# Kernel tuning notes

Measured on AMD Instinct MI355X. Metric: run time of the kernel, lower is better.

The kernel has to match this reference:

```python
import jax, jax.numpy as jnp
from jax import lax
import numpy as np

N = 32768
IN_PLANES = 64
OUT_PLANES = 128
STRIDE = 4
NSAMPLE = 16
EPS = 1e-5


def setup_inputs() -> dict:
    key = jax.random.key(0)
    kp, kx, kw = jax.random.split(key, 3)
    p = jax.random.normal(kp, (N, 3), dtype=jnp.float32)
    x = jax.random.normal(kx, (N, IN_PLANES), dtype=jnp.float32)
    o = jnp.array([N], dtype=jnp.int32)  # batch offsets, passed through unused
    W = jax.random.normal(kw, (3 + IN_PLANES, OUT_PLANES), dtype=jnp.float32) * 0.05
    gamma = jnp.ones((OUT_PLANES,), dtype=jnp.float32)
    beta = jnp.zeros((OUT_PLANES,), dtype=jnp.float32)
    return {"p": p, "x": x, "o": o, "W": W, "gamma": gamma, "beta": beta,
            "stride": STRIDE, "nsample": NSAMPLE}


def fps_indices(p, m):
    # Faithful to the source's furthest_point_sampling: each step picks the
    # argmax of squared distance to the LAST selected point (NOT min over all
    # selected points). Start index fixed to 0 for determinism (source uses a
    # random start).
    def step(last, _):
        d = jnp.sum((p - p[last]) ** 2, axis=1)
        nxt = jnp.argmax(d).astype(jnp.int32)
        return nxt, nxt
    _, rest = lax.scan(step, jnp.int32(0), None, length=m - 1)
    return jnp.concatenate([jnp.zeros((1,), jnp.int32), rest])


def reference(p, x, o, W, gamma, beta, stride, nsample):
    m = p.shape[0] // stride
    fps_idx = fps_indices(p, m)
    new_p = p[fps_idx]                                     # [M,3]

    # exact kNN (KDTree query equivalent): squared euclidean distances [M,N]
    d2 = (jnp.sum(new_p * new_p, axis=1, keepdims=True)
          - 2.0 * new_p @ p.T
          + jnp.sum(p * p, axis=1)[None, :])
    knn = lax.top_k(-lax.stop_gradient(d2), nsample)[1]    # [M,K] nearest indices

    # group: cat(absolute grouped xyz, grouped features) -> [M,K,3+C]
    g = jnp.concatenate([p[knn], x[knn]], axis=-1)
    h = jnp.einsum('mkc,cd->mkd', g, W)                    # linear, [M,K,OUT]

    # BatchNorm1d (training mode, batch statistics) over (M,K) per channel
    mean = jnp.mean(h, axis=(0, 1))
    var = jnp.var(h, axis=(0, 1))
    h = (h - mean) * lax.rsqrt(var + EPS) * gamma + beta
    h = jax.nn.relu(h)

    x_out = jnp.max(h, axis=1)                             # MaxPool1d over nsample
    return new_p, x_out
```

## Files before the change

### kernel.cpp

```cpp
#include <hip/hip_runtime.h>

#define N_PTS 32768
#define M_PTS 8192
#define C_IN  64
#define C_OUT 128
#define KNN   16
#define GDIM  67
#define BN_EPS 1e-5f
#define MAXC  64

#define OFF_FPS   0u
#define OFF_META  32768u
#define OFF_KNN   33024u
#define OFF_CAND  557312u
#define OFF_HBUF  1605888u
#define OFF_UROW  2129920u

typedef unsigned int uint32;
typedef unsigned long long uint64;

__device__ __forceinline__ int slot_count(int s, int nun, int cs, int cl, int M) {
    if (s < cs) return 1;
    const int E = M - nun;
    const int base = E / cl, rem = E % cl;
    const int start = (nun - cs) % cl;
    int off = (s - cs) - start; if (off < 0) off += cl;
    return 1 + base + (off < rem ? 1 : 0);
}

__device__ __forceinline__ uint32 dist_key(float d) {
    uint32 u = __float_as_uint(d);
    return (u & 0x80000000u) ? ~u : (u | 0x80000000u);
}

__global__ void __launch_bounds__(1024) fps_chain_kernel(const float* __restrict__ p,
                                                         int* __restrict__ fps,
                                                         int* __restrict__ meta) {
    __shared__ int   s_chain[M_PTS];
    __shared__ float wv_d[16];
    __shared__ int   wv_i[16];
    __shared__ int s_last, s_done, s_cs, s_win, s_found;
    const int tid  = threadIdx.x;
    const int lane = tid & 63;
    const int wid  = tid >> 6;

    if (tid == 0) { s_chain[0] = 0; s_last = 0; s_done = 0; s_cs = 0; }
    __syncthreads();

    int t = 1;
    while (t < M_PTS) {
        const int last = s_last;
        const float qx = p[3*last], qy = p[3*last+1], qz = p[3*last+2];
        float bd = -1.0f; int bi = 0;
#pragma unroll
        for (int j = 0; j < 32; ++j) {
            const int i = tid + (j << 10);
            float dx = __fsub_rn(p[3*i],   qx);
            float dy = __fsub_rn(p[3*i+1], qy);
            float dz = __fsub_rn(p[3*i+2], qz);
            float d  = __fadd_rn(__fadd_rn(__fmul_rn(dx,dx), __fmul_rn(dy,dy)),
                                 __fmul_rn(dz,dz));
            if (d > bd) { bd = d; bi = i; }
        }
#pragma unroll
        for (int off = 32; off > 0; off >>= 1) {
            float od = __shfl_xor(bd, off);
            int   oi = __shfl_xor(bi, off);
            if (od > bd || (od == bd && oi < bi)) { bd = od; bi = oi; }
        }
        if (lane == 0) { wv_d[wid] = bd; wv_i[wid] = bi; }
        __syncthreads();
        if (wid == 0) {
            float rd = (lane < 16) ? wv_d[lane] : -1.0f;
            int   ri = (lane < 16) ? wv_i[lane] : 0x7fffffff;
#pragma unroll
            for (int off = 8; off > 0; off >>= 1) {
                float od = __shfl_xor(rd, off);
                int   oi = __shfl_xor(ri, off);
                if (od > rd || (od == rd && oi < ri)) { rd = od; ri = oi; }
            }
            if (lane == 0) { s_win = ri; s_found = -1; }
        }
        __syncthreads();
        const int nxt = s_win;
        for (int i = tid; i < t; i += 1024)
            if (s_chain[i] == nxt) s_found = i;
        __syncthreads();
        if (tid == 0) {
            if (s_found >= 0) { s_cs = s_found; s_done = 1; }
            else { s_chain[t] = nxt; s_last = nxt; }
        }
        __syncthreads();
        if (s_done) break;
        ++t;
    }

    if (tid == 0) {
        if (s_done) { meta[0] = t; meta[1] = s_cs; meta[2] = t - s_cs; }
        else        { meta[0] = M_PTS; meta[1] = 0; meta[2] = 1; }
    }
    const int nun = s_done ? t : M_PTS;
    for (int i = tid; i < nun; i += 1024) fps[i] = s_chain[i];
}

__global__ void __launch_bounds__(1024) knn_part_kernel(const float* __restrict__ p,
                                                        const int* __restrict__ fps,
                                                        const int* __restrict__ meta,
                                                        uint64* __restrict__ cand,
                                                        float* __restrict__ newp) {
    const int tid   = threadIdx.x;
    const int lane  = tid & 63;
    const int wid   = tid >> 6;
    const int slice = blockIdx.x & 7;
    const int c0    = blockIdx.x >> 3;
    const int nun   = meta[0];
    const int cs    = meta[1], cl = meta[2];

    for (int e = blockIdx.x * 1024 + tid; e < M_PTS; e += gridDim.x * 1024) {
        const int sl = (e < nun) ? e : cs + (e - cs) % cl;
        const int id = fps[sl];
        newp[3*e]   = p[3*id];
        newp[3*e+1] = p[3*id+1];
        newp[3*e+2] = p[3*id+2];
    }

    for (int c = c0; c < nun && c < MAXC; c += 16) {
        const int cpt = fps[c];
        const float qx = p[3*cpt], qy = p[3*cpt+1], qz = p[3*cpt+2];
        const int base = slice << 12;

        uint64 pk4[4];
#pragma unroll
        for (int j = 0; j < 4; ++j) {
            const int i = base + tid + (j << 10);
            float dx = p[3*i]   - qx;
            float dy = p[3*i+1] - qy;
            float dz = p[3*i+2] - qz;
            float d  = fmaf(dx, dx, fmaf(dy, dy, dz*dz));
            pk4[j] = ((uint64)dist_key(d) << 32) | (uint32)i;
        }

        uint64 lastv = 0ull;
        uint64* out = cand + ((size_t)c << 11) + (slice << 8) + (wid << 4);
        for (int r = 0; r < KNN; ++r) {
            uint64 m = ~0ull;
#pragma unroll
            for (int j = 0; j < 4; ++j) {
                const uint64 v = pk4[j];
                if (v > lastv && v < m) m = v;
            }
#pragma unroll
            for (int off = 32; off > 0; off >>= 1) {
                uint64 o = __shfl_xor(m, off);
                if (o < m) m = o;
            }
            if (lane == 0) out[r] = m;
            lastv = m;
        }
    }
}

__global__ void __launch_bounds__(128) hstats_kernel(const float* __restrict__ p,
                                                     const float* __restrict__ x,
                                                     const float* __restrict__ W,
                                                     const int* __restrict__ meta,
                                                     const uint64* __restrict__ cand,
                                                     float* __restrict__ hbuf) {
    const int c = blockIdx.x >> 4;
    const int k = blockIdx.x & 15;
    const int nun = meta[0];
    if (c >= nun || c >= MAXC) return;
    const int tid  = threadIdx.x;
    const int lane = tid & 63;
    const int wv   = tid >> 6;

    __shared__ uint64 wmin[2];
    __shared__ uint64 s_win;
    __shared__ float  gbuf[GDIM + 1];

    uint64 kc[16];
    const uint64* src = cand + ((size_t)c << 11);
#pragma unroll
    for (int j = 0; j < 16; ++j) kc[j] = src[tid + (j << 7)];

    uint64 lastv = 0ull;
    for (int r = 0; r <= k; ++r) {
        uint64 m = ~0ull;
#pragma unroll
        for (int j = 0; j < 16; ++j) {
            const uint64 v = kc[j];
            if (v > lastv && v < m) m = v;
        }
#pragma unroll
        for (int off = 32; off > 0; off >>= 1) {
            uint64 o = __shfl_xor(m, off);
            if (o < m) m = o;
        }
        if (lane == 0) wmin[wv] = m;
        __syncthreads();
        if (tid == 0) s_win = wmin[0] < wmin[1] ? wmin[0] : wmin[1];
        __syncthreads();
        lastv = s_win;
    }
    const int pt = (int)(lastv & 0xFFFFFFFFull);

    if (tid < GDIM) gbuf[tid] = (tid < 3) ? p[3*pt + tid] : x[(pt << 6) + tid - 3];
    __syncthreads();
    float a = 0.f;
#pragma unroll
    for (int cc = 0; cc < GDIM; ++cc)
        a = fmaf(gbuf[cc], W[cc*C_OUT + tid], a);
    hbuf[(size_t)((c << 4) + k)*C_OUT + tid] = a;
}

__global__ void __launch_bounds__(128) finurow_kernel(const float* __restrict__ p,
                                                      const float* __restrict__ x,
                                                      const float* __restrict__ W,
                                                      const float* __restrict__ gamma,
                                                      const float* __restrict__ beta,
                                                      const int* __restrict__ fps,
                                                      const int* __restrict__ meta,
                                                      const float* __restrict__ hbuf,
                                                      int* __restrict__ knn,
                                                      float* __restrict__ urow) {
    const int tid  = threadIdx.x;
    const int lane = tid & 63;
    const int wv   = tid >> 6;
    const int nun  = meta[0], cs = meta[1], cl = meta[2];
    const int cmax = (nun < MAXC) ? nun : MAXC;

    __shared__ uint64 wmin[2];
    __shared__ uint64 s_win;
    __shared__ float  gbuf[GDIM + 1];

    float s_sum = 0.f, s_sq = 0.f;

    for (int c = 0; c < cmax; ++c) {
        float ls = 0.f, lq = 0.f;
        const float* hb = hbuf + ((size_t)c << 4)*C_OUT;
#pragma unroll
        for (int k = 0; k < KNN; ++k) {
            const float a = hb[k*C_OUT + tid];
            ls += a;
            lq = fmaf(a, a, lq);
        }
        const float cf = (float)slot_count(c, nun, cs, cl, M_PTS);
        s_sum = fmaf(cf, ls, s_sum);
        s_sq  = fmaf(cf, lq, s_sq);
    }
    for (int c = MAXC; c < nun; ++c) {
        const int cpt = fps[c];
        const float qx = p[3*cpt], qy = p[3*cpt+1], qz = p[3*cpt+2];
        uint64 lastv = 0ull;
        for (int r = 0; r < KNN; ++r) {
            uint64 m = ~0ull;
            for (int i = tid; i < N_PTS; i += 128) {
                float dx = p[3*i]   - qx;
                float dy = p[3*i+1] - qy;
                float dz = p[3*i+2] - qz;
                float d  = fmaf(dx, dx, fmaf(dy, dy, dz*dz));
                uint64 v = ((uint64)dist_key(d) << 32) | (uint32)i;
                if (v > lastv && v < m) m = v;
            }
#pragma unroll
            for (int off = 32; off > 0; off >>= 1) {
                uint64 o = __shfl_xor(m, off);
                if (o < m) m = o;
            }
            if (lane == 0) wmin[wv] = m;
            __syncthreads();
            if (tid == 0) {
                uint64 w = wmin[0] < wmin[1] ? wmin[0] : wmin[1];
                s_win = w;
                knn[c*KNN + r] = (int)(w & 0xFFFFFFFFull);
            }
            __syncthreads();
            lastv = s_win;
        }
        float ls = 0.f, lq = 0.f;
#pragma unroll
        for (int k = 0; k < KNN; ++k) {
            const int pt = knn[c*KNN + k];
            if (tid < GDIM) gbuf[tid] = (tid < 3) ? p[3*pt + tid]
                                                  : x[(pt << 6) + tid - 3];
            __syncthreads();
            float a = 0.f;
#pragma unroll
            for (int cc = 0; cc < GDIM; ++cc)
                a = fmaf(gbuf[cc], W[cc*C_OUT + tid], a);
            ls += a;
            lq = fmaf(a, a, lq);
            __syncthreads();
        }
        const float cf = (float)slot_count(c, nun, cs, cl, M_PTS);
        s_sum = fmaf(cf, ls, s_sum);
        s_sq  = fmaf(cf, lq, s_sq);
    }

    const float inv  = 1.0f / (float)(M_PTS * KNN);
    const float mean = s_sum * inv;
    const float var  = s_sq * inv - mean*mean;
    const float sc   = gamma[tid] * rsqrtf(var + BN_EPS);
    const float sh   = fmaf(-mean, sc, beta[tid]);

    for (int c = 0; c < cmax; ++c) {
        const float* hb = hbuf + ((size_t)c << 4)*C_OUT;
        float mx = 0.f;
#pragma unroll
        for (int k = 0; k < KNN; ++k)
            mx = fmaxf(mx, fmaf(hb[k*C_OUT + tid], sc, sh));
        urow[(size_t)c*C_OUT + tid] = mx;
    }
    for (int c = MAXC; c < nun; ++c) {
        float mx = 0.f;
#pragma unroll
        for (int k = 0; k < KNN; ++k) {
            const int pt = knn[c*KNN + k];
            if (tid < GDIM) gbuf[tid] = (tid < 3) ? p[3*pt + tid]
                                                  : x[(pt << 6) + tid - 3];
            __syncthreads();
            float a = 0.f;
#pragma unroll
            for (int cc = 0; cc < GDIM; ++cc)
                a = fmaf(gbuf[cc], W[cc*C_OUT + tid], a);
            mx = fmaxf(mx, fmaf(a, sc, sh));
            __syncthreads();
        }
        urow[(size_t)c*C_OUT + tid] = mx;
    }
}

__global__ void __launch_bounds__(256) bcast_kernel(const int* __restrict__ meta,
                                                    const float* __restrict__ urow,
                                                    float* __restrict__ xout) {
    const int nun = meta[0], cs = meta[1], cl = meta[2];
    const int idx = blockIdx.x * 256 + threadIdx.x;
    const int m = idx >> 5;
    if (m >= M_PTS) return;
    const int c4 = idx & 31;
    const int sl = (m < nun) ? m : cs + (m - cs) % cl;
    float4 v = ((const float4*)urow)[(size_t)sl*32 + c4];
    ((float4*)xout)[(size_t)m*32 + c4] = v;
}

extern "C" void kernel_launch(void* const* d_in, const int* in_sizes, int n_in,
                              void* d_out, int out_size, void* d_ws, size_t ws_size,
                              hipStream_t stream) {
    (void)in_sizes; (void)n_in; (void)out_size; (void)ws_size;
    const float* p     = (const float*)d_in[0];
    const float* x     = (const float*)d_in[1];
    const float* W     = (const float*)d_in[3];
    const float* gamma = (const float*)d_in[4];
    const float* beta  = (const float*)d_in[5];

    float* out  = (float*)d_out;
    float* newp = out;
    float* xout = out + M_PTS * 3;

    char* ws = (char*)d_ws;
    int*    fps   = (int*)   (ws + OFF_FPS);
    int*    meta  = (int*)   (ws + OFF_META);
    int*    knn   = (int*)   (ws + OFF_KNN);
    uint64* cand  = (uint64*)(ws + OFF_CAND);
    float*  hbuf  = (float*) (ws + OFF_HBUF);
    float*  urow  = (float*) (ws + OFF_UROW);

    fps_chain_kernel<<<1, 1024, 0, stream>>>(p, fps, meta);
    knn_part_kernel <<<128, 1024, 0, stream>>>(p, fps, meta, cand, newp);
    hstats_kernel   <<<MAXC*KNN, 128, 0, stream>>>(p, x, W, meta, cand, hbuf);
    finurow_kernel  <<<1, 128, 0, stream>>>(p, x, W, gamma, beta, fps, meta,
                                            hbuf, knn, urow);
    bcast_kernel    <<<M_PTS*32/256, 256, 0, stream>>>(meta, urow, xout);
}
```

Baseline: 58.04 us.

## Vectorize point loads and fuse BN-finalize with broadcast into one grid kernel

Measured after the change: 51.87 us. -10.6%, faster.

```diff
diff --git a/kernel.cpp b/kernel.cpp
--- a/kernel.cpp
+++ b/kernel.cpp
@@ -14,7 +14,6 @@
 #define OFF_KNN   33024u
 #define OFF_CAND  557312u
 #define OFF_HBUF  1605888u
-#define OFF_UROW  2129920u
 
 typedef unsigned int uint32;
 typedef unsigned long long uint64;
@@ -43,6 +42,7 @@
     const int tid  = threadIdx.x;
     const int lane = tid & 63;
     const int wid  = tid >> 6;
+    const float4* p4 = (const float4*)p;
 
     if (tid == 0) { s_chain[0] = 0; s_last = 0; s_done = 0; s_cs = 0; }
     __syncthreads();
@@ -53,14 +53,24 @@
         const float qx = p[3*last], qy = p[3*last+1], qz = p[3*last+2];
         float bd = -1.0f; int bi = 0;
 #pragma unroll
-        for (int j = 0; j < 32; ++j) {
-            const int i = tid + (j << 10);
-            float dx = __fsub_rn(p[3*i],   qx);
-            float dy = __fsub_rn(p[3*i+1], qy);
-            float dz = __fsub_rn(p[3*i+2], qz);
-            float d  = __fadd_rn(__fadd_rn(__fmul_rn(dx,dx), __fmul_rn(dy,dy)),
-                                 __fmul_rn(dz,dz));
-            if (d > bd) { bd = d; bi = i; }
+        for (int j = 0; j < 8; ++j) {
+            const int u = (j << 10) + tid;
+            const int b = u << 2;
+            const float4 f0 = p4[3*u];
+            const float4 f1 = p4[3*u + 1];
+            const float4 f2 = p4[3*u + 2];
+            const float xs[4] = {f0.x, f0.w, f1.z, f2.y};
+            const float ys[4] = {f0.y, f1.x, f1.w, f2.z};
+            const float zs[4] = {f0.z, f1.y, f2.x, f2.w};
+#pragma unroll
+            for (int q = 0; q < 4; ++q) {
+                float dx = __fsub_rn(xs[q], qx);
+                float dy = __fsub_rn(ys[q], qy);
+                float dz = __fsub_rn(zs[q], qz);
+                float d  = __fadd_rn(__fadd_rn(__fmul_rn(dx,dx), __fmul_rn(dy,dy)),
+                                     __fmul_rn(dz,dz));
+                if (d > bd) { bd = d; bi = b + q; }
+            }
         }
 #pragma unroll
         for (int off = 32; off > 0; off >>= 1) {
@@ -115,6 +125,7 @@
     const int c0    = blockIdx.x >> 3;
     const int nun   = meta[0];
     const int cs    = meta[1], cl = meta[2];
+    const float4* p4 = (const float4*)p;
 
     for (int e = blockIdx.x * 1024 + tid; e < M_PTS; e += gridDim.x * 1024) {
         const int sl = (e < nun) ? e : cs + (e - cs) % cl;
@@ -127,17 +138,21 @@
     for (int c = c0; c < nun && c < MAXC; c += 16) {
         const int cpt = fps[c];
         const float qx = p[3*cpt], qy = p[3*cpt+1], qz = p[3*cpt+2];
-        const int base = slice << 12;
+        const int bp = (slice << 12) + (tid << 2);
+        const int u0 = (slice * 3072) + 3*tid;
+        const float4 f0 = p4[u0], f1 = p4[u0+1], f2 = p4[u0+2];
+        const float xs[4] = {f0.x, f0.w, f1.z, f2.y};
+        const float ys[4] = {f0.y, f1.x, f1.w, f2.z};
+        const float zs[4] = {f0.z, f1.y, f2.x, f2.w};
 
         uint64 pk4[4];
 #pragma unroll
-        for (int j = 0; j < 4; ++j) {
-            const int i = base + tid + (j << 10);
-            float dx = p[3*i]   - qx;
-            float dy = p[3*i+1] - qy;
-            float dz = p[3*i+2] - qz;
+        for (int q = 0; q < 4; ++q) {
+            float dx = xs[q] - qx;
+            float dy = ys[q] - qy;
+            float dz = zs[q] - qz;
             float d  = fmaf(dx, dx, fmaf(dy, dy, dz*dz));
-            pk4[j] = ((uint64)dist_key(d) << 32) | (uint32)i;
+            pk4[q] = ((uint64)dist_key(d) << 32) | (uint32)(bp + q);
         }
 
         uint64 lastv = 0ull;
@@ -145,8 +160,8 @@
         for (int r = 0; r < KNN; ++r) {
             uint64 m = ~0ull;
 #pragma unroll
-            for (int j = 0; j < 4; ++j) {
-                const uint64 v = pk4[j];
+            for (int q = 0; q < 4; ++q) {
+                const uint64 v = pk4[q];
                 if (v > lastv && v < m) m = v;
             }
 #pragma unroll
@@ -213,40 +228,41 @@
     hbuf[(size_t)((c << 4) + k)*C_OUT + tid] = a;
 }
 
-__global__ void __launch_bounds__(128) finurow_kernel(const float* __restrict__ p,
-                                                      const float* __restrict__ x,
-                                                      const float* __restrict__ W,
-                                                      const float* __restrict__ gamma,
-                                                      const float* __restrict__ beta,
-                                                      const int* __restrict__ fps,
-                                                      const int* __restrict__ meta,
-                                                      const float* __restrict__ hbuf,
-                                                      int* __restrict__ knn,
-                                                      float* __restrict__ urow) {
-    const int tid  = threadIdx.x;
-    const int lane = tid & 63;
-    const int wv   = tid >> 6;
-    const int nun  = meta[0], cs = meta[1], cl = meta[2];
+__global__ void __launch_bounds__(256) outall_kernel(const float* __restrict__ p,
+                                                     const float* __restrict__ x,
+                                                     const float* __restrict__ W,
+                                                     const float* __restrict__ gamma,
+                                                     const float* __restrict__ beta,
+                                                     const int* __restrict__ fps,
+                                                     const int* __restrict__ meta,
+                                                     const float* __restrict__ hbuf,
+                                                     int* __restrict__ knn,
+                                                     float* __restrict__ xout) {
+    const int tid = threadIdx.x;
+    const int blk = blockIdx.x;
+    const int nun = meta[0], cs = meta[1], cl = meta[2];
     const int cmax = (nun < MAXC) ? nun : MAXC;
 
-    __shared__ uint64 wmin[2];
+    __shared__ float  ssc[128], ssh[128];
+    __shared__ float  gbuf[GDIM + 1];
+    __shared__ uint64 wred[4];
     __shared__ uint64 s_win;
-    __shared__ float  gbuf[GDIM + 1];
 
     float s_sum = 0.f, s_sq = 0.f;
-
-    for (int c = 0; c < cmax; ++c) {
-        float ls = 0.f, lq = 0.f;
-        const float* hb = hbuf + ((size_t)c << 4)*C_OUT;
-#pragma unroll
-        for (int k = 0; k < KNN; ++k) {
-            const float a = hb[k*C_OUT + tid];
-            ls += a;
-            lq = fmaf(a, a, lq);
-        }
-        const float cf = (float)slot_count(c, nun, cs, cl, M_PTS);
-        s_sum = fmaf(cf, ls, s_sum);
-        s_sq  = fmaf(cf, lq, s_sq);
+    if (tid < 128) {
+        for (int c = 0; c < cmax; ++c) {
+            const float* hb = hbuf + ((size_t)c << 4)*C_OUT;
+            float ls = 0.f, lq = 0.f;
+#pragma unroll
+            for (int k = 0; k < KNN; ++k) {
+                const float a = hb[k*C_OUT + tid];
+                ls += a;
+                lq = fmaf(a, a, lq);
+            }
+            const float cf = (float)slot_count(c, nun, cs, cl, M_PTS);
+            s_sum = fmaf(cf, ls, s_sum);
+            s_sq  = fmaf(cf, lq, s_sq);
+        }
     }
     for (int c = MAXC; c < nun; ++c) {
         const int cpt = fps[c];
@@ -254,7 +270,7 @@
         uint64 lastv = 0ull;
         for (int r = 0; r < KNN; ++r) {
             uint64 m = ~0ull;
-            for (int i = tid; i < N_PTS; i += 128) {
+            for (int i = tid; i < N_PTS; i += 256) {
                 float dx = p[3*i]   - qx;
                 float dy = p[3*i+1] - qy;
                 float dz = p[3*i+2] - qz;
@@ -267,12 +283,15 @@
                 uint64 o = __shfl_xor(m, off);
                 if (o < m) m = o;
             }
-            if (lane == 0) wmin[wv] = m;
+            if ((tid & 63) == 0) wred[tid >> 6] = m;
             __syncthreads();
             if (tid == 0) {
-                uint64 w = wmin[0] < wmin[1] ? wmin[0] : wmin[1];
+                uint64 w = wred[0];
+                if (wred[1] < w) w = wred[1];
+                if (wred[2] < w) w = wred[2];
+                if (wred[3] < w) w = wred[3];
                 s_win = w;
-                knn[c*KNN + r] = (int)(w & 0xFFFFFFFFull);
+                knn[(size_t)c*KNN + r] = (int)(w & 0xFFFFFFFFull);
             }
             __syncthreads();
             lastv = s_win;
@@ -280,67 +299,77 @@
         float ls = 0.f, lq = 0.f;
 #pragma unroll
         for (int k = 0; k < KNN; ++k) {
-            const int pt = knn[c*KNN + k];
+            const int pt = knn[(size_t)c*KNN + k];
             if (tid < GDIM) gbuf[tid] = (tid < 3) ? p[3*pt + tid]
                                                   : x[(pt << 6) + tid - 3];
             __syncthreads();
-            float a = 0.f;
-#pragma unroll
-            for (int cc = 0; cc < GDIM; ++cc)
-                a = fmaf(gbuf[cc], W[cc*C_OUT + tid], a);
-            ls += a;
-            lq = fmaf(a, a, lq);
+            if (tid < 128) {
+                float a = 0.f;
+#pragma unroll
+                for (int cc = 0; cc < GDIM; ++cc)
+                    a = fmaf(gbuf[cc], W[cc*C_OUT + tid], a);
+                ls += a;
+                lq = fmaf(a, a, lq);
+            }
             __syncthreads();
         }
-        const float cf = (float)slot_count(c, nun, cs, cl, M_PTS);
-        s_sum = fmaf(cf, ls, s_sum);
-        s_sq  = fmaf(cf, lq, s_sq);
-    }
-
-    const float inv  = 1.0f / (float)(M_PTS * KNN);
-    const float mean = s_sum * inv;
-    const float var  = s_sq * inv - mean*mean;
-    const float sc   = gamma[tid] * rsqrtf(var + BN_EPS);
-    const float sh   = fmaf(-mean, sc, beta[tid]);
-
-    for (int c = 0; c < cmax; ++c) {
-        const float* hb = hbuf + ((size_t)c << 4)*C_OUT;
-        float mx = 0.f;
-#pragma unroll
-        for (int k = 0; k < KNN; ++k)
-            mx = fmaxf(mx, fmaf(hb[k*C_OUT + tid], sc, sh));
-        urow[(size_t)c*C_OUT + tid] = mx;
-    }
-    for (int c = MAXC; c < nun; ++c) {
-        float mx = 0.f;
-#pragma unroll
-        for (int k = 0; k < KNN; ++k) {
-            const int pt = knn[c*KNN + k];
-            if (tid < GDIM) gbuf[tid] = (tid < 3) ? p[3*pt + tid]
-                                                  : x[(pt << 6) + tid - 3];
-            __syncthreads();
-            float a = 0.f;
-#pragma unroll
-            for (int cc = 0; cc < GDIM; ++cc)
-                a = fmaf(gbuf[cc], W[cc*C_OUT + tid], a);
-            mx = fmaxf(mx, fmaf(a, sc, sh));
-            __syncthreads();
-        }
-        urow[(size_t)c*C_OUT + tid] = mx;
-    }
-}
-
-__global__ void __launch_bounds__(256) bcast_kernel(const int* __restrict__ meta,
-                                                    const float* __restrict__ urow,
-                                                    float* __restrict__ xout) {
-    const int nun = meta[0], cs = meta[1], cl = meta[2];
-    const int idx = blockIdx.x * 256 + threadIdx.x;
-    const int m = idx >> 5;
-    if (m >= M_PTS) return;
-    const int c4 = idx & 31;
-    const int sl = (m < nun) ? m : cs + (m - cs) % cl;
-    float4 v = ((const float4*)urow)[(size_t)sl*32 + c4];
-    ((float4*)xout)[(size_t)m*32 + c4] = v;
+        if (tid < 128) {
+            const float cf = (float)slot_count(c, nun, cs, cl, M_PTS);
+            s_sum = fmaf(cf, ls, s_sum);
+            s_sq  = fmaf(cf, lq, s_sq);
+        }
+    }
+    if (tid < 128) {
+        const float inv  = 1.0f / (float)(M_PTS * KNN);
+        const float mean = s_sum * inv;
+        const float var  = s_sq * inv - mean*mean;
+        const float sc   = gamma[tid] * rsqrtf(var + BN_EPS);
+        ssc[tid] = sc;
+        ssh[tid] = fmaf(-mean, sc, beta[tid]);
+    }
+    __syncthreads();
+
+#pragma unroll
+    for (int it = 0; it < 2; ++it) {
+        const int slot = it*256 + tid;
+        const int m  = (blk << 4) + (slot >> 5);
+        const int c4 = slot & 31;
+        const int sl = (m < nun) ? m : cs + (m - cs) % cl;
+        float4 o;
+        float* ov = (float*)&o;
+        if (sl < MAXC) {
+            const float* hb = hbuf + ((size_t)sl << 4)*C_OUT;
+#pragma unroll
+            for (int cc = 0; cc < 4; ++cc) {
+                const int ch = c4*4 + cc;
+                const float sc = ssc[ch], sh = ssh[ch];
+                float mx = 0.f;
+#pragma unroll
+                for (int k = 0; k < KNN; ++k)
+                    mx = fmaxf(mx, fmaf(hb[k*C_OUT + ch], sc, sh));
+                ov[cc] = mx;
+            }
+        } else {
+#pragma unroll
+            for (int cc = 0; cc < 4; ++cc) {
+                const int ch = c4*4 + cc;
+                const float sc = ssc[ch], sh = ssh[ch];
+                float mx = 0.f;
+                for (int k = 0; k < KNN; ++k) {
+                    const int pt = knn[(size_t)sl*KNN + k];
+                    float a = 0.f;
+                    a = fmaf(p[3*pt],   W[0*C_OUT + ch], a);
+                    a = fmaf(p[3*pt+1], W[1*C_OUT + ch], a);
+                    a = fmaf(p[3*pt+2], W[2*C_OUT + ch], a);
+                    for (int cx = 0; cx < C_IN; ++cx)
+                        a = fmaf(x[(pt << 6) + cx], W[(3+cx)*C_OUT + ch], a);
+                    mx = fmaxf(mx, fmaf(a, sc, sh));
+                }
+                ov[cc] = mx;
+            }
+        }
+        ((float4*)xout)[(size_t)m*32 + c4] = o;
+    }
 }
 
 extern "C" void kernel_launch(void* const* d_in, const int* in_sizes, int n_in,
@@ -363,12 +392,10 @@
     int*    knn   = (int*)   (ws + OFF_KNN);
     uint64* cand  = (uint64*)(ws + OFF_CAND);
     float*  hbuf  = (float*) (ws + OFF_HBUF);
-    float*  urow  = (float*) (ws + OFF_UROW);
 
     fps_chain_kernel<<<1, 1024, 0, stream>>>(p, fps, meta);
     knn_part_kernel <<<128, 1024, 0, stream>>>(p, fps, meta, cand, newp);
     hstats_kernel   <<<MAXC*KNN, 128, 0, stream>>>(p, x, W, meta, cand, hbuf);
-    finurow_kernel  <<<1, 128, 0, stream>>>(p, x, W, gamma, beta, fps, meta,
-                                            hbuf, knn, urow);
-    bcast_kernel    <<<M_PTS*32/256, 256, 0, stream>>>(meta, urow, xout);
-}
+    outall_kernel   <<<M_PTS/16, 256, 0, stream>>>(p, x, W, gamma, beta, fps,
+                                                   meta, hbuf, knn, xout);
+}
```
